# Kernel optimization log

Hardware: AMD Instinct MI355X
Metric: run time of the kernel (lower is better)

The kernel has to match this reference:

```python
import jax, jax.numpy as jnp
import numpy as np

N = 50000      # nodes
E = 800000     # edges per etype
IN, HID, OUT = 128, 128, 64
NH = 4         # heads in layerMH
NE = 2         # interaction edge types
NEG = 0.2      # GATConv leaky_relu negative slope


def _gat(x, src, dst, W, al, ar, b, heads, fdim):
    """DGL GATConv (residual=False, activation=None, bias=True).
    x: (N, in); W: (in, heads*fdim); al/ar: (heads, fdim); b: (heads*fdim,)
    Returns (N, heads, fdim)."""
    n = x.shape[0]
    z = (x @ W).reshape(n, heads, fdim)              # (N,H,F)
    el = jnp.sum(z * al, axis=-1)                    # (N,H)
    er = jnp.sum(z * ar, axis=-1)                    # (N,H)
    e = jax.nn.leaky_relu(el[src] + er[dst], NEG)    # (E,H)
    # edge softmax over incoming edges of each dst node
    m = jax.ops.segment_max(e, dst, num_segments=n)
    m = jnp.where(jnp.isfinite(m), m, 0.0)           # zero in-degree safety
    ex = jnp.exp(e - m[dst])
    den = jax.ops.segment_sum(ex, dst, num_segments=n)
    alpha = ex / jnp.maximum(den[dst], 1e-9)         # (E,H)
    out = jax.ops.segment_sum(alpha[:, :, None] * z[src], dst, num_segments=n)
    return out + b.reshape(1, heads, fdim)


def setup_inputs() -> dict:
    key = jax.random.key(0)
    ks = jax.random.split(key, 19)
    x = jax.random.normal(ks[0], (N, IN), jnp.float32)
    src0 = jax.random.randint(ks[1], (E,), 0, N, jnp.int32)
    dst0 = jax.random.randint(ks[2], (E,), 0, N, jnp.int32)
    src1 = jax.random.randint(ks[3], (E,), 0, N, jnp.int32)
    dst1 = jax.random.randint(ks[4], (E,), 0, N, jnp.int32)
    # per-etype GAT params (stacked over the NE edge types)
    W1 = jax.random.normal(ks[5], (NE, IN, HID), jnp.float32) / np.sqrt(IN)
    a_l1 = jax.random.normal(ks[6], (NE, 1, HID), jnp.float32) * 0.1
    a_r1 = jax.random.normal(ks[7], (NE, 1, HID), jnp.float32) * 0.1
    b1 = jnp.zeros((NE, HID), jnp.float32)
    W2 = jax.random.normal(ks[8], (NE, HID, OUT), jnp.float32) / np.sqrt(HID)
    a_l2 = jax.random.normal(ks[9], (NE, 1, OUT), jnp.float32) * 0.1
    a_r2 = jax.random.normal(ks[10], (NE, 1, OUT), jnp.float32) * 0.1
    b2 = jnp.zeros((NE, OUT), jnp.float32)
    Wm = jax.random.normal(ks[11], (NE, OUT, NH * OUT), jnp.float32) / np.sqrt(OUT)
    a_lm = jax.random.normal(ks[12], (NE, NH, OUT), jnp.float32) * 0.1
    a_rm = jax.random.normal(ks[13], (NE, NH, OUT), jnp.float32) * 0.1
    bm = jnp.zeros((NE, NH * OUT), jnp.float32)
    fc_w = jax.random.normal(ks[14], (NE, NE), jnp.float32) * (np.sqrt(2.0) / np.sqrt(NE))
    return dict(x=x, src0=src0, dst0=dst0, src1=src1, dst1=dst1,
                W1=W1, a_l1=a_l1, a_r1=a_r1, b1=b1,
                W2=W2, a_l2=a_l2, a_r2=a_r2, b2=b2,
                Wm=Wm, a_lm=a_lm, a_rm=a_rm, bm=bm, fc_w=fc_w)


def reference(x, src0, dst0, src1, dst1, W1, a_l1, a_r1, b1,
              W2, a_l2, a_r2, b2, Wm, a_lm, a_rm, bm, fc_w):
    srcs, dsts = (src0, src1), (dst0, dst1)
    # layer1: HeteroGraphConv mean over edge types, single head -> (N, HID)
    h1 = jnp.mean(jnp.stack([
        _gat(x, srcs[i], dsts[i], W1[i], a_l1[i], a_r1[i], b1[i], 1, HID)[:, 0, :]
        for i in range(NE)]), axis=0)
    # layer2: agg_func = fc over stacked etype axis, then mean -> (N, OUT)
    h2s = jnp.stack([
        _gat(h1, srcs[i], dsts[i], W2[i], a_l2[i], a_r2[i], b2[i], 1, OUT)[:, 0, :]
        for i in range(NE)], axis=-1)                       # (N, OUT, NE)
    h2 = jnp.mean(jnp.einsum('noe,fe->nof', h2s, fc_w), axis=-1)
    # multi-head layer: mean over edge types -> (N, NH, OUT)
    hm = jnp.mean(jnp.stack([
        _gat(h2, srcs[i], dsts[i], Wm[i], a_lm[i], a_rm[i], bm[i], NH, OUT)
        for i in range(NE)]), axis=0)
    # per-head mean-centering over nodes (vectorized over heads)
    return hm - jnp.mean(hm, axis=0, keepdims=True)
```

## Files before the change

kernel.cpp:

```cpp
#include <hip/hip_runtime.h>

#define NN 50000
#define EE 800000

using short8v = __attribute__((ext_vector_type(8))) short;
using f32x4 = __attribute__((ext_vector_type(4))) float;

__device__ inline unsigned int bf_pack(float lo, float hi) {
  unsigned int a = __float_as_uint(lo);
  a += 0x7FFFu + ((a >> 16) & 1u);
  unsigned int b = __float_as_uint(hi);
  b += 0x7FFFu + ((b >> 16) & 1u);
  return (a >> 16) | ((b >> 16) << 16);
}
__device__ inline void bf_dec8(uint4 v, float* f) {
  f[0] = __uint_as_float(v.x << 16); f[1] = __uint_as_float(v.x & 0xFFFF0000u);
  f[2] = __uint_as_float(v.y << 16); f[3] = __uint_as_float(v.y & 0xFFFF0000u);
  f[4] = __uint_as_float(v.z << 16); f[5] = __uint_as_float(v.z & 0xFFFF0000u);
  f[6] = __uint_as_float(v.w << 16); f[7] = __uint_as_float(v.w & 0xFFFF0000u);
}
__device__ inline float lrelu(float v) { return v >= 0.f ? v : 0.2f * v; }

__device__ inline void split_pack8(const float* v, uint4& h, uint4& l) {
  unsigned int hb[8], lb[8];
  #pragma unroll
  for (int j = 0; j < 8; j++) {
    unsigned int b = __float_as_uint(v[j]);
    hb[j] = b & 0xFFFF0000u;
    float r = v[j] - __uint_as_float(hb[j]);
    lb[j] = __float_as_uint(r) & 0xFFFF0000u;
  }
  h.x = (hb[0] >> 16) | hb[1]; h.y = (hb[2] >> 16) | hb[3];
  h.z = (hb[4] >> 16) | hb[5]; h.w = (hb[6] >> 16) | hb[7];
  l.x = (lb[0] >> 16) | lb[1]; l.y = (lb[2] >> 16) | lb[3];
  l.z = (lb[4] >> 16) | lb[5]; l.w = (lb[6] >> 16) | lb[7];
}

#define SC_BPR 256

__global__ __launch_bounds__(256) void deg2_k(
    const int* __restrict__ dst0, const int* __restrict__ dst1,
    int* __restrict__ deg) {
  const int range = blockIdx.x & 7;
  const int bpr = blockIdx.x >> 3;
  const int lo = range * 6250;
  const int hi = lo + 6250;
  #pragma unroll
  for (int e = 0; e < 2; e++) {
    const int* ds = e ? dst1 : dst0;
    int* dg = deg + e * 50000;
    for (int i = bpr * 256 + threadIdx.x; i < EE; i += SC_BPR * 256) {
      int d = ds[i];
      if (d >= lo && d < hi) atomicAdd(&dg[d], 1);
    }
  }
}

__global__ __launch_bounds__(512) void scan1_k(const int* __restrict__ deg,
                                               int* __restrict__ inc,
                                               int* __restrict__ bsum) {
  __shared__ int s[512];
  int e = blockIdx.y;
  int t = threadIdx.x, i = blockIdx.x * 512 + t;
  int v = (i < NN) ? deg[e * 50000 + i] : 0;
  s[t] = v; __syncthreads();
  #pragma unroll
  for (int off = 1; off < 512; off <<= 1) {
    int u = (t >= off) ? s[t - off] : 0;
    __syncthreads();
    s[t] += u;
    __syncthreads();
  }
  if (i < NN) inc[e * 50000 + i] = s[t];
  if (t == 511) bsum[e * 128 + blockIdx.x] = s[511];
}

__global__ __launch_bounds__(128) void scan2_k(int* __restrict__ bsum, int nb) {
  __shared__ int s[128];
  int e = blockIdx.x;
  int t = threadIdx.x;
  int v = (t < nb) ? bsum[e * 128 + t] : 0;
  s[t] = v; __syncthreads();
  #pragma unroll
  for (int off = 1; off < 128; off <<= 1) {
    int u = (t >= off) ? s[t - off] : 0;
    __syncthreads();
    s[t] += u;
    __syncthreads();
  }
  if (t < nb) bsum[e * 128 + t] = s[t] - v;
}

__global__ __launch_bounds__(256) void scan3_k(const int* __restrict__ deg,
                                               const int* __restrict__ inc,
                                               const int* __restrict__ bsum,
                                               int* __restrict__ rowptr,
                                               int* __restrict__ cursor) {
  int e = blockIdx.y;
  int i = blockIdx.x * 256 + threadIdx.x;
  if (i < NN) {
    int v = inc[e * 50000 + i] - deg[e * 50000 + i] + bsum[e * 128 + (i >> 9)];
    rowptr[e * 50001 + i] = v;
    cursor[e * 50000 + i] = v;
  }
  if (i == NN) rowptr[e * 50001 + NN] = EE;
}

__global__ __launch_bounds__(256) void csr_scatter2_k(
    const int* __restrict__ src0, const int* __restrict__ dst0,
    const int* __restrict__ src1, const int* __restrict__ dst1,
    int* __restrict__ cursor, int* __restrict__ csr_src) {
  const int range = blockIdx.x & 7;
  const int bpr = blockIdx.x >> 3;
  const int lo = range * 6250;
  const int hi = lo + 6250;
  #pragma unroll
  for (int e = 0; e < 2; e++) {
    const int* ds = e ? dst1 : dst0;
    const int* ss = e ? src1 : src0;
    int* cur = cursor + e * 50000;
    int* outp = csr_src + (size_t)e * EE;
    for (int i = bpr * 256 + threadIdx.x; i < EE; i += SC_BPR * 256) {
      int d = ds[i];
      if (d >= lo && d < hi) {
        int pos = atomicAdd(&cur[d], 1);
        outp[pos] = ss[i];
      }
    }
  }
}

__global__ __launch_bounds__(256) void fold_k(
    const float* __restrict__ W1, const float* __restrict__ al1, const float* __restrict__ ar1,
    const float* __restrict__ W2, const float* __restrict__ al2, const float* __restrict__ ar2,
    const float* __restrict__ Wm, const float* __restrict__ alm, const float* __restrict__ arm,
    float* __restrict__ wl1, float* __restrict__ wr1,
    float* __restrict__ wl2, float* __restrict__ wr2,
    float* __restrict__ wlm, float* __restrict__ wrm) {
  int t = blockIdx.x * 256 + threadIdx.x;
  if (t < 512) {
    int lr = t >> 8, e = (t >> 7) & 1, k = t & 127;
    const float* a = (lr ? ar1 : al1) + e * 128;
    const float* w = W1 + ((size_t)e * 128 + k) * 128;
    float s = 0.f;
    for (int f = 0; f < 128; f++) s += w[f] * a[f];
    (lr ? wr1 : wl1)[e * 128 + k] = s;
  } else if (t < 1024) {
    int u = t - 512;
    int lr = u >> 8, e = (u >> 7) & 1, k = u & 127;
    const float* a = (lr ? ar2 : al2) + e * 64;
    const float* w = W2 + ((size_t)e * 128 + k) * 64;
    float s = 0.f;
    for (int f = 0; f < 64; f++) s += w[f] * a[f];
    (lr ? wr2 : wl2)[e * 128 + k] = s;
  } else if (t < 2048) {
    int u = t - 1024;
    int lr = u >> 9, e = (u >> 8) & 1, h = (u >> 6) & 3, k = u & 63;
    const float* a = (lr ? arm : alm) + (e * 4 + h) * 64;
    const float* w = Wm + ((size_t)e * 64 + k) * 256 + h * 64;
    float s = 0.f;
    for (int f = 0; f < 64; f++) s += w[f] * a[f];
    (lr ? wrm : wlm)[(e * 4 + h) * 64 + k] = s;
  }
}

__global__ __launch_bounds__(256) void wtrans_k(
    const float* __restrict__ W1, const float* __restrict__ W2,
    const float* __restrict__ Wm,
    unsigned short* __restrict__ w1h, unsigned short* __restrict__ w1l,
    unsigned short* __restrict__ w2h, unsigned short* __restrict__ w2l,
    unsigned short* __restrict__ wmh, unsigned short* __restrict__ wml) {
  int t = blockIdx.x * 256 + threadIdx.x;
  float v; unsigned short *ph, *pl; int oi;
  if (t < 32768) {
    int j = t & 7, n = (t >> 3) & 127, kg = (t >> 10) & 15, e = t >> 14;
    v = W1[((size_t)(e * 128 + kg * 8 + j)) * 128 + n];
    ph = w1h; pl = w1l; oi = t;
  } else if (t < 49152) {
    int i = t - 32768;
    int j = i & 7, n = (i >> 3) & 63, kg = (i >> 9) & 15, e = i >> 13;
    v = W2[((size_t)(e * 128 + kg * 8 + j)) * 64 + n];
    ph = w2h; pl = w2l; oi = i;
  } else if (t < 81920) {
    int i = t - 49152;
    int j = i & 7, n = (i >> 3) & 255, kg = (i >> 11) & 7, e = i >> 14;
    v = Wm[((size_t)(e * 64 + kg * 8 + j)) * 256 + n];
    ph = wmh; pl = wml; oi = i;
  } else return;
  unsigned int b = __float_as_uint(v);
  unsigned int hb = b & 0xFFFF0000u;
  float r = v - __uint_as_float(hb);
  unsigned int lb = __float_as_uint(r);
  ph[oi] = (unsigned short)(hb >> 16);
  pl[oi] = (unsigned short)(lb >> 16);
}

__global__ __launch_bounds__(256) void xdot_k(
    const float* __restrict__ x, const float* __restrict__ wl,
    const float* __restrict__ wr, unsigned int* __restrict__ xb,
    float* __restrict__ el, float* __restrict__ er) {
  int n = blockIdx.x * 16 + (threadIdx.x >> 4);
  int lane = threadIdx.x & 15;
  if (n >= NN) return;
  float p[4] = {0.f, 0.f, 0.f, 0.f};
  #pragma unroll
  for (int i = 0; i < 2; i++) {
    int c = (lane + i * 16) * 4;
    float4 xv = *(const float4*)(x + (size_t)n * 128 + c);
    uint2 o;
    o.x = bf_pack(xv.x, xv.y);
    o.y = bf_pack(xv.z, xv.w);
    *(uint2*)(xb + (size_t)n * 64 + c / 2) = o;
    #pragma unroll
    for (int e = 0; e < 2; e++) {
      float4 a = *(const float4*)(wl + e * 128 + c);
      float4 b = *(const float4*)(wr + e * 128 + c);
      p[e*2+0] += xv.x*a.x + xv.y*a.y + xv.z*a.z + xv.w*a.w;
      p[e*2+1] += xv.x*b.x + xv.y*b.y + xv.z*b.z + xv.w*b.w;
    }
  }
  #pragma unroll
  for (int off = 1; off < 16; off <<= 1) {
    #pragma unroll
    for (int i = 0; i < 4; i++) p[i] += __shfl_xor(p[i], off);
  }
  if (lane == 0) {
    el[n] = p[0]; er[n] = p[1];
    el[NN + n] = p[2]; er[NN + n] = p[3];
  }
}

__global__ __launch_bounds__(256) void agg_x_f(
    const int* __restrict__ rowptr, const int* __restrict__ csr_src,
    const float* __restrict__ el, const float* __restrict__ er,
    const uint4* __restrict__ xb, float* __restrict__ u1) {
  int d = blockIdx.x * 16 + (threadIdx.x >> 4);
  int lane = threadIdx.x & 15;
  if (d >= NN) return;
  #pragma unroll
  for (int e = 0; e < 2; e++) {
    const int* rp = rowptr + e * 50001;
    const int* cs = csr_src + (size_t)e * EE;
    const float* elp = el + (size_t)e * NN;
    float erd = er[(size_t)e * NN + d];
    int j0 = rp[d], j1 = rp[d + 1];
    float sm = 0.f;
    float acc[8] = {};
    int j = j0;
    for (; j + 16 <= j1; j += 16) {
      int sl = cs[j + lane];
      float al = __expf(lrelu(elp[sl] + erd));
      sm += al;
      #pragma unroll
      for (int k = 0; k < 16; k++) {
        int s = __shfl(sl, k, 16);
        float a = __shfl(al, k, 16);
        uint4 xv = xb[(size_t)s * 16 + lane];
        float f[8]; bf_dec8(xv, f);
        #pragma unroll
        for (int c = 0; c < 8; c++) acc[c] += a * f[c];
      }
    }
    int r = j1 - j;
    if (r > 0) {
      int jj = j + (lane < r ? lane : 0);
      int sl = cs[jj];
      float al = __expf(lrelu(elp[sl] + erd));
      if (lane < r) sm += al;
      for (int k = 0; k < r; k++) {
        int s = __shfl(sl, k, 16);
        float a = __shfl(al, k, 16);
        uint4 xv = xb[(size_t)s * 16 + lane];
        float f[8]; bf_dec8(xv, f);
        #pragma unroll
        for (int c = 0; c < 8; c++) acc[c] += a * f[c];
      }
    }
    #pragma unroll
    for (int off = 1; off < 16; off <<= 1) sm += __shfl_xor(sm, off, 16);
    float inv = 1.f / fmaxf(sm, 1e-9f);
    float* up = u1 + ((size_t)e * NN + d) * 128 + lane * 8;
    *(float4*)up       = make_float4(acc[0]*inv, acc[1]*inv, acc[2]*inv, acc[3]*inv);
    *(float4*)(up + 4) = make_float4(acc[4]*inv, acc[5]*inv, acc[6]*inv, acc[7]*inv);
  }
}

__global__ __launch_bounds__(256) void layer12_k(
    const float* __restrict__ u1, const unsigned short* __restrict__ w1h,
    const unsigned short* __restrict__ w1l, const float* __restrict__ b1,
    const unsigned short* __restrict__ w2h, const unsigned short* __restrict__ w2l,
    const float* __restrict__ wl2, const float* __restrict__ wr2,
    unsigned int* __restrict__ Zb, float* __restrict__ el,
    float* __restrict__ er) {
  __shared__ float smem[128 * 132];
  uint4* AsH = (uint4*)smem;
  uint4* AsL = AsH + 512;
  float* Hs = smem;
  const int tid = threadIdx.x;
  const int row0 = blockIdx.x * 128;
  const int wv = tid >> 6, lane = tid & 63;
  const int l15 = lane & 15, lg = lane >> 4;
  const uint4* b1h4 = (const uint4*)w1h;
  const uint4* b1l4 = (const uint4*)w1l;
  const uint4* b2h4 = (const uint4*)w2h;
  const uint4* b2l4 = (const uint4*)w2l;

  f32x4 acc[2][8] = {};
  for (int e = 0; e < 2; e++) {
    const float* Ap = u1 + (size_t)e * NN * 128;
    for (int k0 = 0; k0 < 128; k0 += 32) {
      {
        int r = tid & 127, half = tid >> 7;
        int rr = row0 + r; if (rr >= NN) rr = NN - 1;
        const float* ap = Ap + (size_t)rr * 128 + k0;
        #pragma unroll
        for (int i = 0; i < 2; i++) {
          int kg = half * 2 + i;
          float4 a0 = *(const float4*)(ap + kg * 8);
          float4 a1 = *(const float4*)(ap + kg * 8 + 4);
          float v[8] = {a0.x, a0.y, a0.z, a0.w, a1.x, a1.y, a1.z, a1.w};
          uint4 hh, ll;
          split_pack8(v, hh, ll);
          AsH[kg * 128 + r] = hh;
          AsL[kg * 128 + r] = ll;
        }
      }
      __syncthreads();
      short8v ah[2], al[2];
      #pragma unroll
      for (int mf = 0; mf < 2; mf++) {
        int slot = lg * 128 + wv * 32 + mf * 16 + l15;
        ah[mf] = *reinterpret_cast<const short8v*>(&AsH[slot]);
        al[mf] = *reinterpret_cast<const short8v*>(&AsL[slot]);
      }
      int kgb = e * 16 + (k0 >> 3) + lg;
      #pragma unroll
      for (int nf = 0; nf < 8; nf++) {
        int bslot = kgb * 128 + nf * 16 + l15;
        short8v bh = *reinterpret_cast<const short8v*>(&b1h4[bslot]);
        short8v bl = *reinterpret_cast<const short8v*>(&b1l4[bslot]);
        #pragma unroll
        for (int mf = 0; mf < 2; mf++) {
          acc[mf][nf] = __builtin_amdgcn_mfma_f32_16x16x32_bf16(ah[mf], bh, acc[mf][nf], 0, 0, 0);
          acc[mf][nf] = __builtin_amdgcn_mfma_f32_16x16x32_bf16(al[mf], bh, acc[mf][nf], 0, 0, 0);
          acc[mf][nf] = __builtin_amdgcn_mfma_f32_16x16x32_bf16(ah[mf], bl, acc[mf][nf], 0, 0, 0);
        }
      }
      __syncthreads();
    }
  }
  #pragma unroll
  for (int nf = 0; nf < 8; nf++) {
    int col = nf * 16 + l15;
    float bb = 0.5f * (b1[col] + b1[128 + col]);
    #pragma unroll
    for (int mf = 0; mf < 2; mf++) {
      #pragma unroll
      for (int reg = 0; reg < 4; reg++) {
        int rloc = wv * 32 + mf * 16 + lg * 4 + reg;
        Hs[rloc * 132 + col] = 0.5f * acc[mf][nf][reg] + bb;
      }
    }
  }
  __syncthreads();
  {
    int r = tid >> 1, half = tid & 1;
    int grow = row0 + r;
    const float* hrow = Hs + r * 132 + half * 64;
    float p0 = 0.f, p1 = 0.f, p2 = 0.f, p3 = 0.f;
    #pragma unroll 8
    for (int c = 0; c < 64; c++) {
      float hv = hrow[c];
      int k = half * 64 + c;
      p0 += hv * wl2[k];       p1 += hv * wr2[k];
      p2 += hv * wl2[128 + k]; p3 += hv * wr2[128 + k];
    }
    p0 += __shfl_xor(p0, 1); p1 += __shfl_xor(p1, 1);
    p2 += __shfl_xor(p2, 1); p3 += __shfl_xor(p3, 1);
    if (!half && grow < NN) {
      el[grow] = p0;      er[grow] = p1;
      el[NN + grow] = p2; er[NN + grow] = p3;
    }
  }
  f32x4 acc2[2][2][4] = {};
  for (int k0 = 0; k0 < 128; k0 += 32) {
    short8v ah[2], al[2];
    #pragma unroll
    for (int mf = 0; mf < 2; mf++) {
      int ra = wv * 32 + mf * 16 + l15;
      const float* hp = Hs + ra * 132 + k0 + lg * 8;
      float4 h0 = *(const float4*)hp;
      float4 h1v = *(const float4*)(hp + 4);
      float v[8] = {h0.x, h0.y, h0.z, h0.w, h1v.x, h1v.y, h1v.z, h1v.w};
      uint4 hh, ll;
      split_pack8(v, hh, ll);
      ah[mf] = *reinterpret_cast<const short8v*>(&hh);
      al[mf] = *reinterpret_cast<const short8v*>(&ll);
    }
    #pragma unroll
    for (int e = 0; e < 2; e++) {
      int kgb = e * 16 + (k0 >> 3) + lg;
      #pragma unroll
      for (int nf = 0; nf < 4; nf++) {
        int bslot = kgb * 64 + nf * 16 + l15;
        short8v bh = *reinterpret_cast<const short8v*>(&b2h4[bslot]);
        short8v bl = *reinterpret_cast<const short8v*>(&b2l4[bslot]);
        #pragma unroll
        for (int mf = 0; mf < 2; mf++) {
          acc2[e][mf][nf] = __builtin_amdgcn_mfma_f32_16x16x32_bf16(ah[mf], bh, acc2[e][mf][nf], 0, 0, 0);
          acc2[e][mf][nf] = __builtin_amdgcn_mfma_f32_16x16x32_bf16(al[mf], bh, acc2[e][mf][nf], 0, 0, 0);
          acc2[e][mf][nf] = __builtin_amdgcn_mfma_f32_16x16x32_bf16(ah[mf], bl, acc2[e][mf][nf], 0, 0, 0);
        }
      }
    }
  }
  #pragma unroll
  for (int e = 0; e < 2; e++) {
    #pragma unroll
    for (int mf = 0; mf < 2; mf++) {
      #pragma unroll
      for (int nf = 0; nf < 4; nf++) {
        #pragma unroll
        for (int reg = 0; reg < 4; reg++) {
          float v = acc2[e][mf][nf][reg];
          float nb = __shfl_xor(v, 1);
          int row = row0 + wv * 32 + mf * 16 + lg * 4 + reg;
          if (!(lane & 1) && row < NN) {
            Zb[((size_t)e * NN + row) * 32 + nf * 8 + (l15 >> 1)] = bf_pack(v, nb);
          }
        }
      }
    }
  }
}

__global__ __launch_bounds__(256) void agg2_f(
    const int* __restrict__ rowptr, const int* __restrict__ csr_src,
    const float* __restrict__ el, const float* __restrict__ er,
    const uint4* __restrict__ zb, const float* __restrict__ bias,
    const float* __restrict__ fcw, const float* __restrict__ wlm,
    const float* __restrict__ wrm, uint4* __restrict__ h2b,
    float* __restrict__ elm, float* __restrict__ erm) {
  int d = blockIdx.x * 32 + (threadIdx.x >> 3);
  int lane = threadIdx.x & 7;
  if (d >= NN) return;
  int c0 = lane * 8;
  float coef0 = 0.5f * (fcw[0] + fcw[2]);
  float coef1 = 0.5f * (fcw[1] + fcw[3]);
  float hrow[8];
  #pragma unroll
  for (int c = 0; c < 8; c++)
    hrow[c] = coef0 * bias[c0 + c] + coef1 * bias[64 + c0 + c];
  #pragma unroll
  for (int e = 0; e < 2; e++) {
    const int* rp = rowptr + e * 50001;
    const int* cs = csr_src + (size_t)e * EE;
    const float* elp = el + (size_t)e * NN;
    float erd = er[(size_t)e * NN + d];
    const uint4* zp = zb + (size_t)e * NN * 8;
    int j0 = rp[d], j1 = rp[d + 1];
    float sm = 0.f;
    float acc[8] = {};
    int j = j0;
    for (; j + 8 <= j1; j += 8) {
      int sl = cs[j + lane];
      float al = __expf(lrelu(elp[sl] + erd));
      sm += al;
      #pragma unroll
      for (int k = 0; k < 8; k++) {
        int s = __shfl(sl, k, 8);
        float a = __shfl(al, k, 8);
        uint4 zv = zp[(size_t)s * 8 + lane];
        float f[8]; bf_dec8(zv, f);
        #pragma unroll
        for (int c = 0; c < 8; c++) acc[c] += a * f[c];
      }
    }
    int r = j1 - j;
    if (r > 0) {
      int jj = j + (lane < r ? lane : 0);
      int sl = cs[jj];
      float al = __expf(lrelu(elp[sl] + erd));
      if (lane < r) sm += al;
      for (int k = 0; k < r; k++) {
        int s = __shfl(sl, k, 8);
        float a = __shfl(al, k, 8);
        uint4 zv = zp[(size_t)s * 8 + lane];
        float f[8]; bf_dec8(zv, f);
        #pragma unroll
        for (int c = 0; c < 8; c++) acc[c] += a * f[c];
      }
    }
    #pragma unroll
    for (int off = 1; off < 8; off <<= 1) sm += __shfl_xor(sm, off, 8);
    float cinv = (e ? coef1 : coef0) / fmaxf(sm, 1e-9f);
    #pragma unroll
    for (int c = 0; c < 8; c++) hrow[c] += cinv * acc[c];
  }
  uint4 o;
  o.x = bf_pack(hrow[0], hrow[1]); o.y = bf_pack(hrow[2], hrow[3]);
  o.z = bf_pack(hrow[4], hrow[5]); o.w = bf_pack(hrow[6], hrow[7]);
  h2b[(size_t)d * 8 + lane] = o;
  float p[16];
  #pragma unroll
  for (int e2 = 0; e2 < 2; e2++) {
    #pragma unroll
    for (int h = 0; h < 4; h++) {
      const float* a = wlm + (e2 * 4 + h) * 64 + c0;
      const float* b = wrm + (e2 * 4 + h) * 64 + c0;
      float sl = 0.f, sr = 0.f;
      #pragma unroll
      for (int c = 0; c < 8; c++) { sl += hrow[c] * a[c]; sr += hrow[c] * b[c]; }
      p[e2*4+h] = sl; p[8+e2*4+h] = sr;
    }
  }
  #pragma unroll
  for (int off = 1; off < 8; off <<= 1) {
    #pragma unroll
    for (int i = 0; i < 16; i++) p[i] += __shfl_xor(p[i], off, 8);
  }
  if (lane == 0) *(float4*)(elm + (size_t)d * 4)        = make_float4(p[0], p[1], p[2], p[3]);
  if (lane == 1) *(float4*)(elm + ((size_t)NN + d) * 4) = make_float4(p[4], p[5], p[6], p[7]);
  if (lane == 2) *(float4*)(erm + (size_t)d * 4)        = make_float4(p[8], p[9], p[10], p[11]);
  if (lane == 3) *(float4*)(erm + ((size_t)NN + d) * 4) = make_float4(p[12], p[13], p[14], p[15]);
}

__global__ __launch_bounds__(256) void agg_mh_k(
    const int* __restrict__ rowptr, const int* __restrict__ csr_src,
    const float* __restrict__ elm, const float* __restrict__ erm,
    const uint4* __restrict__ h2b, float* __restrict__ u) {
  int d = blockIdx.x * 32 + (threadIdx.x >> 3);
  int lane = threadIdx.x & 7, c0 = lane * 8;
  if (d >= NN) return;
  #pragma unroll
  for (int e = 0; e < 2; e++) {
    const int* rp = rowptr + e * 50001;
    const int* cs = csr_src + (size_t)e * EE;
    const float* elp = elm + (size_t)e * NN * 4;
    float4 er4 = *(const float4*)(erm + ((size_t)e * NN + d) * 4);
    int j0 = rp[d], j1 = rp[d + 1];
    float4 sm = make_float4(0.f, 0.f, 0.f, 0.f);
    float acc[4][8] = {};
    int j = j0;
    for (; j + 2 <= j1; j += 2) {
      int sA = cs[j], sB = cs[j+1];
      float4 vA = *(const float4*)(elp + (size_t)sA * 4);
      float4 vB = *(const float4*)(elp + (size_t)sB * 4);
      uint4 hA = h2b[(size_t)sA * 8 + lane];
      uint4 hB = h2b[(size_t)sB * 8 + lane];
      float4 wA, wB;
      wA.x = __expf(lrelu(vA.x + er4.x));
      wA.y = __expf(lrelu(vA.y + er4.y));
      wA.z = __expf(lrelu(vA.z + er4.z));
      wA.w = __expf(lrelu(vA.w + er4.w));
      wB.x = __expf(lrelu(vB.x + er4.x));
      wB.y = __expf(lrelu(vB.y + er4.y));
      wB.z = __expf(lrelu(vB.z + er4.z));
      wB.w = __expf(lrelu(vB.w + er4.w));
      sm.x += wA.x + wB.x; sm.y += wA.y + wB.y;
      sm.z += wA.z + wB.z; sm.w += wA.w + wB.w;
      float fA[8], fB[8];
      bf_dec8(hA, fA); bf_dec8(hB, fB);
      #pragma unroll
      for (int c = 0; c < 8; c++) {
        acc[0][c] += wA.x*fA[c] + wB.x*fB[c];
        acc[1][c] += wA.y*fA[c] + wB.y*fB[c];
        acc[2][c] += wA.z*fA[c] + wB.z*fB[c];
        acc[3][c] += wA.w*fA[c] + wB.w*fB[c];
      }
    }
    for (; j < j1; j++) {
      int s = cs[j];
      float4 v = *(const float4*)(elp + (size_t)s * 4);
      uint4 hh = h2b[(size_t)s * 8 + lane];
      float4 w;
      w.x = __expf(lrelu(v.x + er4.x));
      w.y = __expf(lrelu(v.y + er4.y));
      w.z = __expf(lrelu(v.z + er4.z));
      w.w = __expf(lrelu(v.w + er4.w));
      sm.x += w.x; sm.y += w.y; sm.z += w.z; sm.w += w.w;
      float f[8]; bf_dec8(hh, f);
      #pragma unroll
      for (int c = 0; c < 8; c++) {
        acc[0][c] += w.x*f[c]; acc[1][c] += w.y*f[c];
        acc[2][c] += w.z*f[c]; acc[3][c] += w.w*f[c];
      }
    }
    float4 inv = make_float4(1.f / fmaxf(sm.x, 1e-9f), 1.f / fmaxf(sm.y, 1e-9f),
                             1.f / fmaxf(sm.z, 1e-9f), 1.f / fmaxf(sm.w, 1e-9f));
    float iv[4] = {inv.x, inv.y, inv.z, inv.w};
    #pragma unroll
    for (int h = 0; h < 4; h++) {
      float* up = u + (((size_t)(e * 4 + h) * NN) + d) * 64 + c0;
      *(float4*)up       = make_float4(acc[h][0]*iv[h], acc[h][1]*iv[h],
                                       acc[h][2]*iv[h], acc[h][3]*iv[h]);
      *(float4*)(up + 4) = make_float4(acc[h][4]*iv[h], acc[h][5]*iv[h],
                                       acc[h][6]*iv[h], acc[h][7]*iv[h]);
    }
  }
}

__global__ __launch_bounds__(256) void colsum_u_k(
    const float* __restrict__ u, float* __restrict__ usum) {
  __shared__ float lds[4][64];
  int eh = blockIdx.x >> 6;
  int chunk = blockIdx.x & 63;
  int c = threadIdx.x & 63, rg = threadIdx.x >> 6;
  const float* up = u + (size_t)eh * NN * 64;
  int n0 = chunk * 782;
  int n1 = n0 + 782; if (n1 > NN) n1 = NN;
  float s = 0.f;
  for (int n = n0 + rg; n < n1; n += 4) s += up[(size_t)n * 64 + c];
  lds[rg][c] = s;
  __syncthreads();
  if (rg == 0) {
    float t = lds[0][c] + lds[1][c] + lds[2][c] + lds[3][c];
    unsafeAtomicAdd(&usum[eh * 64 + c], t);
  }
}

__global__ __launch_bounds__(256) void mean_k(
    const float* __restrict__ usum, const float* __restrict__ Wm,
    float* __restrict__ mean) {
  int c = threadIdx.x;
  int h = c >> 6;
  float s = 0.f;
  for (int e = 0; e < 2; e++) {
    const float* us = usum + (e * 4 + h) * 64;
    const float* wp = Wm + (size_t)e * 64 * 256 + c;
    for (int k = 0; k < 64; k++) s += us[k] * wp[(size_t)k * 256];
  }
  mean[c] = s * (0.5f / NN);
}

__global__ __launch_bounds__(256) void out_gemm_k(
    const float* __restrict__ u, const unsigned short* __restrict__ wmh,
    const unsigned short* __restrict__ wml, const float* __restrict__ mean,
    float* __restrict__ out) {
  __shared__ uint4 AsH[512], AsL[512];
  const int h = blockIdx.y;
  const int tid = threadIdx.x;
  const int row0 = blockIdx.x * 128;
  const int wv = tid >> 6, lane = tid & 63;
  const int l15 = lane & 15, lg = lane >> 4;
  f32x4 acc[2][4] = {};
  const uint4* bh4 = (const uint4*)wmh;
  const uint4* bl4 = (const uint4*)wml;
  for (int e = 0; e < 2; e++) {
    const float* Ap = u + (size_t)(e * 4 + h) * NN * 64;
    for (int k0 = 0; k0 < 64; k0 += 32) {
      {
        int r = tid & 127, half = tid >> 7;
        int rr = row0 + r; if (rr >= NN) rr = NN - 1;
        const float* ap = Ap + (size_t)rr * 64 + k0;
        #pragma unroll
        for (int i = 0; i < 2; i++) {
          int kg = half * 2 + i;
          float4 a0 = *(const float4*)(ap + kg * 8);
          float4 a1 = *(const float4*)(ap + kg * 8 + 4);
          float v[8] = {a0.x, a0.y, a0.z, a0.w, a1.x, a1.y, a1.z, a1.w};
          uint4 hh, ll;
          split_pack8(v, hh, ll);
          AsH[kg * 128 + r] = hh;
          AsL[kg * 128 + r] = ll;
        }
      }
      __syncthreads();
      short8v ah[2], al[2];
      #pragma unroll
      for (int mf = 0; mf < 2; mf++) {
        int slot = lg * 128 + wv * 32 + mf * 16 + l15;
        ah[mf] = *reinterpret_cast<const short8v*>(&AsH[slot]);
        al[mf] = *reinterpret_cast<const short8v*>(&AsL[slot]);
      }
      int kgb = e * 8 + (k0 >> 3) + lg;
      #pragma unroll
      for (int nf = 0; nf < 4; nf++) {
        int bslot = kgb * 256 + h * 64 + nf * 16 + l15;
        short8v bh = *reinterpret_cast<const short8v*>(&bh4[bslot]);
        short8v bl = *reinterpret_cast<const short8v*>(&bl4[bslot]);
        #pragma unroll
        for (int mf = 0; mf < 2; mf++) {
          acc[mf][nf] = __builtin_amdgcn_mfma_f32_16x16x32_bf16(ah[mf], bh, acc[mf][nf], 0, 0, 0);
          acc[mf][nf] = __builtin_amdgcn_mfma_f32_16x16x32_bf16(al[mf], bh, acc[mf][nf], 0, 0, 0);
          acc[mf][nf] = __builtin_amdgcn_mfma_f32_16x16x32_bf16(ah[mf], bl, acc[mf][nf], 0, 0, 0);
        }
      }
      __syncthreads();
    }
  }
  #pragma unroll
  for (int nf = 0; nf < 4; nf++) {
    int col = nf * 16 + l15;
    float mn = mean[h * 64 + col];
    #pragma unroll
    for (int mf = 0; mf < 2; mf++) {
      #pragma unroll
      for (int reg = 0; reg < 4; reg++) {
        int row = row0 + wv * 32 + mf * 16 + lg * 4 + reg;
        if (row < NN)
          out[(size_t)row * 256 + h * 64 + col] = 0.5f * acc[mf][nf][reg] - mn;
      }
    }
  }
}

extern "C" void kernel_launch(void* const* d_in, const int* in_sizes, int n_in,
                              void* d_out, int out_size, void* d_ws, size_t ws_size,
                              hipStream_t stream) {
  const float* x  = (const float*)d_in[0];
  const int* src0 = (const int*)d_in[1];
  const int* dst0 = (const int*)d_in[2];
  const int* src1 = (const int*)d_in[3];
  const int* dst1 = (const int*)d_in[4];
  const float* W1  = (const float*)d_in[5];
  const float* al1 = (const float*)d_in[6];
  const float* ar1 = (const float*)d_in[7];
  const float* b1  = (const float*)d_in[8];
  const float* W2  = (const float*)d_in[9];
  const float* al2 = (const float*)d_in[10];
  const float* ar2 = (const float*)d_in[11];
  const float* b2  = (const float*)d_in[12];
  const float* Wm  = (const float*)d_in[13];
  const float* alm = (const float*)d_in[14];
  const float* arm = (const float*)d_in[15];
  const float* fcw = (const float*)d_in[17];
  float* out = (float*)d_out;

  float* ws = (float*)d_ws;
  float* zu     = ws;
  unsigned int* z2b = (unsigned int*)(ws + 12800000);
  unsigned int* xb = (unsigned int*)(ws + 25600000);
  unsigned int* h2b = (unsigned int*)(ws + 32000000);
  float* el     = ws + 33600000;
  float* er     = ws + 34000000;
  float* elm    = ws + 34400000;
  float* erm    = ws + 34800000;
  float* wl1    = ws + 35200000;
  float* wr1    = wl1 + 256;
  float* wl2    = wr1 + 256;
  float* wr2    = wl2 + 256;
  float* wlm    = wr2 + 256;
  float* wrm    = wlm + 512;
  float* usum   = wrm + 512;
  float* meanp  = usum + 512;
  int* rowptr  = (int*)(meanp + 256);
  int* csr_src = rowptr + 100002;
  unsigned short* w1h = (unsigned short*)(csr_src + 2 * EE + 2);
  unsigned short* w1l = w1h + 32768;
  unsigned short* w2h = w1l + 32768;
  unsigned short* w2l = w2h + 16384;
  unsigned short* wmh = w2l + 16384;
  unsigned short* wml = wmh + 32768;
  int* deg    = (int*)el;
  int* inc    = (int*)er;
  int* cursor = (int*)zu;
  int* bsum   = (int*)zu + 200000;

  hipMemsetAsync(deg, 0, 2 * 50000 * sizeof(int), stream);
  hipMemsetAsync(usum, 0, 512 * sizeof(float), stream);
  deg2_k<<<8 * SC_BPR, 256, 0, stream>>>(dst0, dst1, deg);
  scan1_k<<<dim3(98, 2), 512, 0, stream>>>(deg, inc, bsum);
  scan2_k<<<2, 128, 0, stream>>>(bsum, 98);
  scan3_k<<<dim3(196, 2), 256, 0, stream>>>(deg, inc, bsum, rowptr, cursor);
  csr_scatter2_k<<<8 * SC_BPR, 256, 0, stream>>>(src0, dst0, src1, dst1,
                                                 cursor, csr_src);

  fold_k<<<8, 256, 0, stream>>>(W1, al1, ar1, W2, al2, ar2, Wm, alm, arm,
                                wl1, wr1, wl2, wr2, wlm, wrm);
  wtrans_k<<<320, 256, 0, stream>>>(W1, W2, Wm, w1h, w1l, w2h, w2l, wmh, wml);

  xdot_k<<<3125, 256, 0, stream>>>(x, wl1, wr1, xb, el, er);
  agg_x_f<<<3125, 256, 0, stream>>>(rowptr, csr_src, el, er, (const uint4*)xb, zu);
  layer12_k<<<391, 256, 0, stream>>>(zu, w1h, w1l, b1, w2h, w2l, wl2, wr2,
                                     z2b, el, er);

  agg2_f<<<1563, 256, 0, stream>>>(rowptr, csr_src, el, er, (const uint4*)z2b,
                                   b2, fcw, wlm, wrm, (uint4*)h2b, elm, erm);

  agg_mh_k<<<1563, 256, 0, stream>>>(rowptr, csr_src, elm, erm,
                                     (const uint4*)h2b, zu);
  colsum_u_k<<<512, 256, 0, stream>>>(zu, usum);
  mean_k<<<1, 256, 0, stream>>>(usum, Wm, meanp);
  out_gemm_k<<<dim3(391, 4), 256, 0, stream>>>(zu, Wm != nullptr ? wmh : wmh, wml, meanp, out);
}
```

Measured before the change: 623.3 us.

## Sub-bucket CSR edges by source range to improve gather locality

The CSR build now keys each edge on (dst, source range of 6250 nodes), giving 8 sub-buckets per destination, so each destination's neighbours come out grouped by source range. The three aggregation kernels walk the 8 sub-buckets in order, which tends to make concurrent warps gather from similar source regions and improves L2 reuse of feature rows. The cost is a degree and scan array eight times larger, extra scan work, and per-bucket loop overhead with more partial 16- or 8-wide remainder chunks in the aggregation loops.

```diff
diff --git a/kernel.cpp b/kernel.cpp
--- a/kernel.cpp
+++ b/kernel.cpp
@@ -2,6 +2,9 @@
 
 #define NN 50000
 #define EE 800000
+#define NR 8
+#define RW 6250
+#define NB 400000
 
 using short8v = __attribute__((ext_vector_type(8))) short;
 using f32x4 = __attribute__((ext_vector_type(4))) float;
@@ -39,19 +42,24 @@
 #define SC_BPR 256
 
 __global__ __launch_bounds__(256) void deg2_k(
-    const int* __restrict__ dst0, const int* __restrict__ dst1,
+    const int* __restrict__ src0, const int* __restrict__ dst0,
+    const int* __restrict__ src1, const int* __restrict__ dst1,
     int* __restrict__ deg) {
   const int range = blockIdx.x & 7;
   const int bpr = blockIdx.x >> 3;
-  const int lo = range * 6250;
-  const int hi = lo + 6250;
+  const int lo = range * RW;
+  const int hi = lo + RW;
   #pragma unroll
   for (int e = 0; e < 2; e++) {
     const int* ds = e ? dst1 : dst0;
-    int* dg = deg + e * 50000;
+    const int* ss = e ? src1 : src0;
+    int* dg = deg + e * NB;
     for (int i = bpr * 256 + threadIdx.x; i < EE; i += SC_BPR * 256) {
       int d = ds[i];
-      if (d >= lo && d < hi) atomicAdd(&dg[d], 1);
+      if (d >= lo && d < hi) {
+        int s = ss[i];
+        atomicAdd(&dg[(d << 3) | (s / RW)], 1);
+      }
     }
   }
 }
@@ -62,7 +70,7 @@
   __shared__ int s[512];
   int e = blockIdx.y;
   int t = threadIdx.x, i = blockIdx.x * 512 + t;
-  int v = (i < NN) ? deg[e * 50000 + i] : 0;
+  int v = (i < NB) ? deg[e * NB + i] : 0;
   s[t] = v; __syncthreads();
   #pragma unroll
   for (int off = 1; off < 512; off <<= 1) {
@@ -71,39 +79,39 @@
     s[t] += u;
     __syncthreads();
   }
-  if (i < NN) inc[e * 50000 + i] = s[t];
-  if (t == 511) bsum[e * 128 + blockIdx.x] = s[511];
-}
-
-__global__ __launch_bounds__(128) void scan2_k(int* __restrict__ bsum, int nb) {
-  __shared__ int s[128];
+  if (i < NB) inc[e * NB + i] = s[t];
+  if (t == 511) bsum[e * 1024 + blockIdx.x] = s[511];
+}
+
+__global__ __launch_bounds__(1024) void scan2_k(int* __restrict__ bsum, int nb) {
+  __shared__ int s[1024];
   int e = blockIdx.x;
   int t = threadIdx.x;
-  int v = (t < nb) ? bsum[e * 128 + t] : 0;
+  int v = (t < nb) ? bsum[e * 1024 + t] : 0;
   s[t] = v; __syncthreads();
   #pragma unroll
-  for (int off = 1; off < 128; off <<= 1) {
+  for (int off = 1; off < 1024; off <<= 1) {
     int u = (t >= off) ? s[t - off] : 0;
     __syncthreads();
     s[t] += u;
     __syncthreads();
   }
-  if (t < nb) bsum[e * 128 + t] = s[t] - v;
+  if (t < nb) bsum[e * 1024 + t] = s[t] - v;
 }
 
 __global__ __launch_bounds__(256) void scan3_k(const int* __restrict__ deg,
                                                const int* __restrict__ inc,
                                                const int* __restrict__ bsum,
-                                               int* __restrict__ rowptr,
+                                               int* __restrict__ srp,
                                                int* __restrict__ cursor) {
   int e = blockIdx.y;
   int i = blockIdx.x * 256 + threadIdx.x;
-  if (i < NN) {
-    int v = inc[e * 50000 + i] - deg[e * 50000 + i] + bsum[e * 128 + (i >> 9)];
-    rowptr[e * 50001 + i] = v;
-    cursor[e * 50000 + i] = v;
-  }
-  if (i == NN) rowptr[e * 50001 + NN] = EE;
+  if (i < NB) {
+    int v = inc[e * NB + i] - deg[e * NB + i] + bsum[e * 1024 + (i >> 9)];
+    srp[e * (NB + 1) + i] = v;
+    cursor[e * NB + i] = v;
+  }
+  if (i == NB) srp[e * (NB + 1) + NB] = EE;
 }
 
 __global__ __launch_bounds__(256) void csr_scatter2_k(
@@ -112,19 +120,20 @@
     int* __restrict__ cursor, int* __restrict__ csr_src) {
   const int range = blockIdx.x & 7;
   const int bpr = blockIdx.x >> 3;
-  const int lo = range * 6250;
-  const int hi = lo + 6250;
+  const int lo = range * RW;
+  const int hi = lo + RW;
   #pragma unroll
   for (int e = 0; e < 2; e++) {
     const int* ds = e ? dst1 : dst0;
     const int* ss = e ? src1 : src0;
-    int* cur = cursor + e * 50000;
+    int* cur = cursor + e * NB;
     int* outp = csr_src + (size_t)e * EE;
     for (int i = bpr * 256 + threadIdx.x; i < EE; i += SC_BPR * 256) {
       int d = ds[i];
       if (d >= lo && d < hi) {
-        int pos = atomicAdd(&cur[d], 1);
-        outp[pos] = ss[i];
+        int s = ss[i];
+        int pos = atomicAdd(&cur[(d << 3) | (s / RW)], 1);
+        outp[pos] = s;
       }
     }
   }
@@ -231,7 +240,7 @@
 }
 
 __global__ __launch_bounds__(256) void agg_x_f(
-    const int* __restrict__ rowptr, const int* __restrict__ csr_src,
+    const int* __restrict__ srp, const int* __restrict__ csr_src,
     const float* __restrict__ el, const float* __restrict__ er,
     const uint4* __restrict__ xb, float* __restrict__ u1) {
   int d = blockIdx.x * 16 + (threadIdx.x >> 4);
@@ -239,41 +248,44 @@
   if (d >= NN) return;
   #pragma unroll
   for (int e = 0; e < 2; e++) {
-    const int* rp = rowptr + e * 50001;
+    const int* bp = srp + (size_t)e * (NB + 1) + ((size_t)d << 3);
     const int* cs = csr_src + (size_t)e * EE;
     const float* elp = el + (size_t)e * NN;
     float erd = er[(size_t)e * NN + d];
-    int j0 = rp[d], j1 = rp[d + 1];
     float sm = 0.f;
     float acc[8] = {};
-    int j = j0;
-    for (; j + 16 <= j1; j += 16) {
-      int sl = cs[j + lane];
-      float al = __expf(lrelu(elp[sl] + erd));
-      sm += al;
-      #pragma unroll
-      for (int k = 0; k < 16; k++) {
-        int s = __shfl(sl, k, 16);
-        float a = __shfl(al, k, 16);
-        uint4 xv = xb[(size_t)s * 16 + lane];
-        float f[8]; bf_dec8(xv, f);
-        #pragma unroll
-        for (int c = 0; c < 8; c++) acc[c] += a * f[c];
-      }
-    }
-    int r = j1 - j;
-    if (r > 0) {
-      int jj = j + (lane < r ? lane : 0);
-      int sl = cs[jj];
-      float al = __expf(lrelu(elp[sl] + erd));
-      if (lane < r) sm += al;
-      for (int k = 0; k < r; k++) {
-        int s = __shfl(sl, k, 16);
-        float a = __shfl(al, k, 16);
-        uint4 xv = xb[(size_t)s * 16 + lane];
-        float f[8]; bf_dec8(xv, f);
-        #pragma unroll
-        for (int c = 0; c < 8; c++) acc[c] += a * f[c];
+    #pragma unroll 1
+    for (int rg = 0; rg < NR; rg++) {
+      int j0 = bp[rg], j1 = bp[rg + 1];
+      int j = j0;
+      for (; j + 16 <= j1; j += 16) {
+        int sl = cs[j + lane];
+        float al = __expf(lrelu(elp[sl] + erd));
+        sm += al;
+        #pragma unroll
+        for (int k = 0; k < 16; k++) {
+          int s = __shfl(sl, k, 16);
+          float a = __shfl(al, k, 16);
+          uint4 xv = xb[(size_t)s * 16 + lane];
+          float f[8]; bf_dec8(xv, f);
+          #pragma unroll
+          for (int c = 0; c < 8; c++) acc[c] += a * f[c];
+        }
+      }
+      int rem = j1 - j;
+      if (rem > 0) {
+        int jj = j + (lane < rem ? lane : 0);
+        int sl = cs[jj];
+        float al = __expf(lrelu(elp[sl] + erd));
+        if (lane < rem) sm += al;
+        for (int k = 0; k < rem; k++) {
+          int s = __shfl(sl, k, 16);
+          float a = __shfl(al, k, 16);
+          uint4 xv = xb[(size_t)s * 16 + lane];
+          float f[8]; bf_dec8(xv, f);
+          #pragma unroll
+          for (int c = 0; c < 8; c++) acc[c] += a * f[c];
+        }
       }
     }
     #pragma unroll
@@ -435,7 +447,7 @@
 }
 
 __global__ __launch_bounds__(256) void agg2_f(
-    const int* __restrict__ rowptr, const int* __restrict__ csr_src,
+    const int* __restrict__ srp, const int* __restrict__ csr_src,
     const float* __restrict__ el, const float* __restrict__ er,
     const uint4* __restrict__ zb, const float* __restrict__ bias,
     const float* __restrict__ fcw, const float* __restrict__ wlm,
@@ -453,42 +465,45 @@
     hrow[c] = coef0 * bias[c0 + c] + coef1 * bias[64 + c0 + c];
   #pragma unroll
   for (int e = 0; e < 2; e++) {
-    const int* rp = rowptr + e * 50001;
+    const int* bp = srp + (size_t)e * (NB + 1) + ((size_t)d << 3);
     const int* cs = csr_src + (size_t)e * EE;
     const float* elp = el + (size_t)e * NN;
     float erd = er[(size_t)e * NN + d];
     const uint4* zp = zb + (size_t)e * NN * 8;
-    int j0 = rp[d], j1 = rp[d + 1];
     float sm = 0.f;
     float acc[8] = {};
-    int j = j0;
-    for (; j + 8 <= j1; j += 8) {
-      int sl = cs[j + lane];
-      float al = __expf(lrelu(elp[sl] + erd));
-      sm += al;
-      #pragma unroll
-      for (int k = 0; k < 8; k++) {
-        int s = __shfl(sl, k, 8);
-        float a = __shfl(al, k, 8);
-        uint4 zv = zp[(size_t)s * 8 + lane];
-        float f[8]; bf_dec8(zv, f);
-        #pragma unroll
-        for (int c = 0; c < 8; c++) acc[c] += a * f[c];
-      }
-    }
-    int r = j1 - j;
-    if (r > 0) {
-      int jj = j + (lane < r ? lane : 0);
-      int sl = cs[jj];
-      float al = __expf(lrelu(elp[sl] + erd));
-      if (lane < r) sm += al;
-      for (int k = 0; k < r; k++) {
-        int s = __shfl(sl, k, 8);
-        float a = __shfl(al, k, 8);
-        uint4 zv = zp[(size_t)s * 8 + lane];
-        float f[8]; bf_dec8(zv, f);
-        #pragma unroll
-        for (int c = 0; c < 8; c++) acc[c] += a * f[c];
+    #pragma unroll 1
+    for (int rg = 0; rg < NR; rg++) {
+      int j0 = bp[rg], j1 = bp[rg + 1];
+      int j = j0;
+      for (; j + 8 <= j1; j += 8) {
+        int sl = cs[j + lane];
+        float al = __expf(lrelu(elp[sl] + erd));
+        sm += al;
+        #pragma unroll
+        for (int k = 0; k < 8; k++) {
+          int s = __shfl(sl, k, 8);
+          float a = __shfl(al, k, 8);
+          uint4 zv = zp[(size_t)s * 8 + lane];
+          float f[8]; bf_dec8(zv, f);
+          #pragma unroll
+          for (int c = 0; c < 8; c++) acc[c] += a * f[c];
+        }
+      }
+      int rem = j1 - j;
+      if (rem > 0) {
+        int jj = j + (lane < rem ? lane : 0);
+        int sl = cs[jj];
+        float al = __expf(lrelu(elp[sl] + erd));
+        if (lane < rem) sm += al;
+        for (int k = 0; k < rem; k++) {
+          int s = __shfl(sl, k, 8);
+          float a = __shfl(al, k, 8);
+          uint4 zv = zp[(size_t)s * 8 + lane];
+          float f[8]; bf_dec8(zv, f);
+          #pragma unroll
+          for (int c = 0; c < 8; c++) acc[c] += a * f[c];
+        }
       }
     }
     #pragma unroll
@@ -526,7 +541,7 @@
 }
 
 __global__ __launch_bounds__(256) void agg_mh_k(
-    const int* __restrict__ rowptr, const int* __restrict__ csr_src,
+    const int* __restrict__ srp, const int* __restrict__ csr_src,
     const float* __restrict__ elm, const float* __restrict__ erm,
     const uint4* __restrict__ h2b, float* __restrict__ u) {
   int d = blockIdx.x * 32 + (threadIdx.x >> 3);
@@ -534,56 +549,59 @@
   if (d >= NN) return;
   #pragma unroll
   for (int e = 0; e < 2; e++) {
-    const int* rp = rowptr + e * 50001;
+    const int* bp = srp + (size_t)e * (NB + 1) + ((size_t)d << 3);
     const int* cs = csr_src + (size_t)e * EE;
     const float* elp = elm + (size_t)e * NN * 4;
     float4 er4 = *(const float4*)(erm + ((size_t)e * NN + d) * 4);
-    int j0 = rp[d], j1 = rp[d + 1];
     float4 sm = make_float4(0.f, 0.f, 0.f, 0.f);
     float acc[4][8] = {};
-    int j = j0;
-    for (; j + 2 <= j1; j += 2) {
-      int sA = cs[j], sB = cs[j+1];
-      float4 vA = *(const float4*)(elp + (size_t)sA * 4);
-      float4 vB = *(const float4*)(elp + (size_t)sB * 4);
-      uint4 hA = h2b[(size_t)sA * 8 + lane];
-      uint4 hB = h2b[(size_t)sB * 8 + lane];
-      float4 wA, wB;
-      wA.x = __expf(lrelu(vA.x + er4.x));
-      wA.y = __expf(lrelu(vA.y + er4.y));
-      wA.z = __expf(lrelu(vA.z + er4.z));
-      wA.w = __expf(lrelu(vA.w + er4.w));
-      wB.x = __expf(lrelu(vB.x + er4.x));
-      wB.y = __expf(lrelu(vB.y + er4.y));
-      wB.z = __expf(lrelu(vB.z + er4.z));
-      wB.w = __expf(lrelu(vB.w + er4.w));
-      sm.x += wA.x + wB.x; sm.y += wA.y + wB.y;
-      sm.z += wA.z + wB.z; sm.w += wA.w + wB.w;
-      float fA[8], fB[8];
-      bf_dec8(hA, fA); bf_dec8(hB, fB);
-      #pragma unroll
-      for (int c = 0; c < 8; c++) {
-        acc[0][c] += wA.x*fA[c] + wB.x*fB[c];
-        acc[1][c] += wA.y*fA[c] + wB.y*fB[c];
-        acc[2][c] += wA.z*fA[c] + wB.z*fB[c];
-        acc[3][c] += wA.w*fA[c] + wB.w*fB[c];
-      }
-    }
-    for (; j < j1; j++) {
-      int s = cs[j];
-      float4 v = *(const float4*)(elp + (size_t)s * 4);
-      uint4 hh = h2b[(size_t)s * 8 + lane];
-      float4 w;
-      w.x = __expf(lrelu(v.x + er4.x));
-      w.y = __expf(lrelu(v.y + er4.y));
-      w.z = __expf(lrelu(v.z + er4.z));
-      w.w = __expf(lrelu(v.w + er4.w));
-      sm.x += w.x; sm.y += w.y; sm.z += w.z; sm.w += w.w;
-      float f[8]; bf_dec8(hh, f);
-      #pragma unroll
-      for (int c = 0; c < 8; c++) {
-        acc[0][c] += w.x*f[c]; acc[1][c] += w.y*f[c];
-        acc[2][c] += w.z*f[c]; acc[3][c] += w.w*f[c];
+    #pragma unroll 1
+    for (int rg = 0; rg < NR; rg++) {
+      int j0 = bp[rg], j1 = bp[rg + 1];
+      int j = j0;
+      for (; j + 2 <= j1; j += 2) {
+        int sA = cs[j], sB = cs[j+1];
+        float4 vA = *(const float4*)(elp + (size_t)sA * 4);
+        float4 vB = *(const float4*)(elp + (size_t)sB * 4);
+        uint4 hA = h2b[(size_t)sA * 8 + lane];
+        uint4 hB = h2b[(size_t)sB * 8 + lane];
+        float4 wA, wB;
+        wA.x = __expf(lrelu(vA.x + er4.x));
+        wA.y = __expf(lrelu(vA.y + er4.y));
+        wA.z = __expf(lrelu(vA.z + er4.z));
+        wA.w = __expf(lrelu(vA.w + er4.w));
+        wB.x = __expf(lrelu(vB.x + er4.x));
+        wB.y = __expf(lrelu(vB.y + er4.y));
+        wB.z = __expf(lrelu(vB.z + er4.z));
+        wB.w = __expf(lrelu(vB.w + er4.w));
+        sm.x += wA.x + wB.x; sm.y += wA.y + wB.y;
+        sm.z += wA.z + wB.z; sm.w += wA.w + wB.w;
+        float fA[8], fB[8];
+        bf_dec8(hA, fA); bf_dec8(hB, fB);
+        #pragma unroll
+        for (int c = 0; c < 8; c++) {
+          acc[0][c] += wA.x*fA[c] + wB.x*fB[c];
+          acc[1][c] += wA.y*fA[c] + wB.y*fB[c];
+          acc[2][c] += wA.z*fA[c] + wB.z*fB[c];
+          acc[3][c] += wA.w*fA[c] + wB.w*fB[c];
+        }
+      }
+      for (; j < j1; j++) {
+        int s = cs[j];
+        float4 v = *(const float4*)(elp + (size_t)s * 4);
+        uint4 hh = h2b[(size_t)s * 8 + lane];
+        float4 w;
+        w.x = __expf(lrelu(v.x + er4.x));
+        w.y = __expf(lrelu(v.y + er4.y));
+        w.z = __expf(lrelu(v.z + er4.z));
+        w.w = __expf(lrelu(v.w + er4.w));
+        sm.x += w.x; sm.y += w.y; sm.z += w.z; sm.w += w.w;
+        float f[8]; bf_dec8(hh, f);
+        #pragma unroll
+        for (int c = 0; c < 8; c++) {
+          acc[0][c] += w.x*f[c]; acc[1][c] += w.y*f[c];
+          acc[2][c] += w.z*f[c]; acc[3][c] += w.w*f[c];
+        }
       }
     }
     float4 inv = make_float4(1.f / fmaxf(sm.x, 1e-9f), 1.f / fmaxf(sm.y, 1e-9f),
@@ -744,25 +762,25 @@
   float* wrm    = wlm + 512;
   float* usum   = wrm + 512;
   float* meanp  = usum + 512;
-  int* rowptr  = (int*)(meanp + 256);
-  int* csr_src = rowptr + 100002;
+  int* srp     = (int*)(meanp + 256);
+  int* csr_src = srp + 2 * (NB + 1);
   unsigned short* w1h = (unsigned short*)(csr_src + 2 * EE + 2);
   unsigned short* w1l = w1h + 32768;
   unsigned short* w2h = w1l + 32768;
   unsigned short* w2l = w2h + 16384;
   unsigned short* wmh = w2l + 16384;
   unsigned short* wml = wmh + 32768;
-  int* deg    = (int*)el;
-  int* inc    = (int*)er;
-  int* cursor = (int*)zu;
-  int* bsum   = (int*)zu + 200000;
-
-  hipMemsetAsync(deg, 0, 2 * 50000 * sizeof(int), stream);
+  int* deg    = (int*)zu;
+  int* inc    = (int*)zu + 2 * NB;
+  int* cursor = (int*)zu + 4 * NB;
+  int* bsum   = (int*)zu + 6 * NB;
+
+  hipMemsetAsync(deg, 0, 2 * NB * sizeof(int), stream);
   hipMemsetAsync(usum, 0, 512 * sizeof(float), stream);
-  deg2_k<<<8 * SC_BPR, 256, 0, stream>>>(dst0, dst1, deg);
-  scan1_k<<<dim3(98, 2), 512, 0, stream>>>(deg, inc, bsum);
-  scan2_k<<<2, 128, 0, stream>>>(bsum, 98);
-  scan3_k<<<dim3(196, 2), 256, 0, stream>>>(deg, inc, bsum, rowptr, cursor);
+  deg2_k<<<8 * SC_BPR, 256, 0, stream>>>(src0, dst0, src1, dst1, deg);
+  scan1_k<<<dim3(782, 2), 512, 0, stream>>>(deg, inc, bsum);
+  scan2_k<<<2, 1024, 0, stream>>>(bsum, 782);
+  scan3_k<<<dim3(1563, 2), 256, 0, stream>>>(deg, inc, bsum, srp, cursor);
   csr_scatter2_k<<<8 * SC_BPR, 256, 0, stream>>>(src0, dst0, src1, dst1,
                                                  cursor, csr_src);
 
@@ -771,16 +789,16 @@
   wtrans_k<<<320, 256, 0, stream>>>(W1, W2, Wm, w1h, w1l, w2h, w2l, wmh, wml);
 
   xdot_k<<<3125, 256, 0, stream>>>(x, wl1, wr1, xb, el, er);
-  agg_x_f<<<3125, 256, 0, stream>>>(rowptr, csr_src, el, er, (const uint4*)xb, zu);
+  agg_x_f<<<3125, 256, 0, stream>>>(srp, csr_src, el, er, (const uint4*)xb, zu);
   layer12_k<<<391, 256, 0, stream>>>(zu, w1h, w1l, b1, w2h, w2l, wl2, wr2,
                                      z2b, el, er);
 
-  agg2_f<<<1563, 256, 0, stream>>>(rowptr, csr_src, el, er, (const uint4*)z2b,
+  agg2_f<<<1563, 256, 0, stream>>>(srp, csr_src, el, er, (const uint4*)z2b,
                                    b2, fcw, wlm, wrm, (uint4*)h2b, elm, erm);
 
-  agg_mh_k<<<1563, 256, 0, stream>>>(rowptr, csr_src, elm, erm,
+  agg_mh_k<<<1563, 256, 0, stream>>>(srp, csr_src, elm, erm,
                                      (const uint4*)h2b, zu);
   colsum_u_k<<<512, 256, 0, stream>>>(zu, usum);
   mean_k<<<1, 256, 0, stream>>>(usum, Wm, meanp);
-  out_gemm_k<<<dim3(391, 4), 256, 0, stream>>>(zu, Wm != nullptr ? wmh : wmh, wml, meanp, out);
-}
+  out_gemm_k<<<dim3(391, 4), 256, 0, stream>>>(zu, wmh, wml, meanp, out);
+}
```

Result: slower. 796.8 us (+27.8%).
